# Kernel tuning notes

Measured on AMD Instinct MI355X. Metric: run time of the kernel, lower is better.

The kernel has to match this reference:

```python
import jax, jax.numpy as jnp
import numpy as np

EPS = 1e-06  # used both as eps and as the F.threshold threshold (mqjs passes eps as th)


def _pair_log_dist_sum(x1, x2, th):
    # dist[i,j] = ||x1_i||^2 + ||x2_j||^2 - 2 x1_i . x2_j  (n x n)
    x1x2 = x1 @ x2.T
    sq1 = jnp.sum(x1 * x1, axis=1)[:, None]
    sq2 = jnp.sum(x2 * x2, axis=1)[None, :]
    dist = sq1 + sq2 - 2.0 * x1x2
    # F.threshold(dist, th, 1): values <= th -> 1; then clamp(min=1), sqrt, log, row-sum
    dist = jnp.where(dist > th, dist, 1.0)
    dist = jnp.maximum(dist, 1.0)
    return jnp.sum(0.5 * jnp.log(dist), axis=1)  # log(sqrt(d)) == 0.5*log(d)


def _mqjs(inp, tgt, eps):
    n = inp.shape[0]
    x1 = inp.reshape(n, -1)
    x2 = tgt.reshape(n, -1)
    p = (x1 + x2) / 2.0
    ce = _pair_log_dist_sum(x1, p, eps) + _pair_log_dist_sum(x2, p, eps)
    se = _pair_log_dist_sum(x1, x1, eps) * (n / (n - 1))
    return jnp.mean(ce - se)


def setup_inputs() -> dict:
    key = jax.random.key(0)
    k1, k2 = jax.random.split(key)
    n, d = 8192, 256
    inp = jax.random.normal(k1, (n, d), dtype=jnp.float32)
    tgt = jax.random.normal(k2, (n, d), dtype=jnp.float32)
    return {"input": inp, "target": tgt}


def reference(input, target):
    return _mqjs(input, target, EPS)
```

## Files before the change

### kernel.cpp

```cpp
#include <hip/hip_runtime.h>

#define N 8192
#define D 256
#define BM 128
#define BJ 64
#define JG 4
#define GJ (N / BJ / JG)
#define GI (N / BM)

typedef int   i32x4 __attribute__((ext_vector_type(4)));
typedef int   i32x8 __attribute__((ext_vector_type(8)));
typedef float f32x4 __attribute__((ext_vector_type(4)));
typedef float f32x2 __attribute__((ext_vector_type(2)));

__device__ __forceinline__ unsigned pack_fp8x4(float a, float b, float c, float d) {
    unsigned lo = __builtin_amdgcn_cvt_pk_fp8_f32(a, b, 0, false);
    return __builtin_amdgcn_cvt_pk_fp8_f32(c, d, lo, true);
}
__device__ __forceinline__ float dequant_sumsq(unsigned q) {
    const float v0 = __builtin_amdgcn_cvt_f32_fp8(q, 0);
    const float v1 = __builtin_amdgcn_cvt_f32_fp8(q, 1);
    const float v2 = __builtin_amdgcn_cvt_f32_fp8(q, 2);
    const float v3 = __builtin_amdgcn_cvt_f32_fp8(q, 3);
    return fmaf(v0, v0, fmaf(v1, v1, fmaf(v2, v2, v3 * v3)));
}

__global__ void prep_kernel(const float* __restrict__ x1, const float* __restrict__ x2,
                            unsigned* __restrict__ x1q, unsigned* __restrict__ x2q,
                            unsigned* __restrict__ pq,
                            float* __restrict__ sq1, float* __restrict__ sq2,
                            float* __restrict__ sqp) {
    const int tid = threadIdx.x, lane = tid & 63, wv = tid >> 6;
    const int row = blockIdx.x * 4 + wv;
    const size_t eb = (size_t)row * D + lane * 4;
    const float4 a = *(const float4*)(x1 + eb);
    const float4 b = *(const float4*)(x2 + eb);
    const float px = 0.5f * (a.x + b.x), py = 0.5f * (a.y + b.y);
    const float pz = 0.5f * (a.z + b.z), pw = 0.5f * (a.w + b.w);
    const unsigned qa = pack_fp8x4(a.x, a.y, a.z, a.w);
    const unsigned qb = pack_fp8x4(b.x, b.y, b.z, b.w);
    const unsigned qp = pack_fp8x4(px, py, pz, pw);
    const size_t wb = (size_t)row * (D / 4) + lane;
    x1q[wb] = qa; x2q[wb] = qb; pq[wb] = qp;
    float s1 = dequant_sumsq(qa), s2 = dequant_sumsq(qb), sp = dequant_sumsq(qp);
    #pragma unroll
    for (int o = 32; o > 0; o >>= 1) {
        s1 += __shfl_down(s1, o, 64);
        s2 += __shfl_down(s2, o, 64);
        sp += __shfl_down(sp, o, 64);
    }
    if (lane == 0) { sq1[row] = s1; sq2[row] = s2; sqp[row] = sp; }
}

__device__ __forceinline__ f32x4 mfma8(i32x8 a, i32x8 b, f32x4 c) {
    return __builtin_amdgcn_mfma_scale_f32_16x16x128_f8f6f4(
        a, b, c, 0, 0, 0, 0x7F7F7F7F, 0, 0x7F7F7F7F);
}

__device__ __forceinline__ i32x8 frag_at(const unsigned char* b, int olo, int ohi) {
    const i32x4 lo = *(const i32x4*)(b + olo);
    const i32x4 hi = *(const i32x4*)(b + ohi);
    i32x8 f;
    f[0] = lo[0]; f[1] = lo[1]; f[2] = lo[2]; f[3] = lo[3];
    f[4] = hi[0]; f[5] = hi[1]; f[6] = hi[2]; f[7] = hi[3];
    return f;
}

__device__ __forceinline__ void stageB8(const unsigned char* __restrict__ g,
                                        unsigned char* s, int rowbase, size_t kb,
                                        int wv, int srow, int sblk) {
    const int row = wv * 8 + srow;
    __builtin_amdgcn_global_load_lds(
        (const __attribute__((address_space(1))) void*)(g + (size_t)(rowbase + row) * D + kb + sblk * 16),
        (__attribute__((address_space(3))) void*)(s + wv * 1024), 16, 0, 0);
}

__device__ __forceinline__ float logsumP(const f32x4 (&acc)[2][2],
                                         const f32x2 (&sa01)[2], const f32x2 (&sa23)[2],
                                         const float sb[2]) {
    float s = 0.0f;
    #pragma unroll
    for (int ti = 0; ti < 2; ++ti) {
        f32x2 pr = {1.0f, 1.0f};
        #pragma unroll
        for (int tj = 0; tj < 2; ++tj) {
            const f32x2 sbv = {sb[tj], sb[tj]};
            const f32x2 t01 = sa01[ti] + sbv, t23 = sa23[ti] + sbv;
            const f32x2 v01 = {acc[ti][tj][0], acc[ti][tj][1]};
            const f32x2 v23 = {acc[ti][tj][2], acc[ti][tj][3]};
            f32x2 d01 = t01 - 2.0f * v01;
            f32x2 d23 = t23 - 2.0f * v23;
            d01 = __builtin_elementwise_max(d01, (f32x2){1.0f, 1.0f});
            d23 = __builtin_elementwise_max(d23, (f32x2){1.0f, 1.0f});
            pr *= d01; pr *= d23;
        }
        s += __log2f(pr.x * pr.y);
    }
    return s;
}

__device__ __forceinline__ float logsumStraddle(const f32x4 (&acc)[2][2],
                                                const f32x2 (&sa01)[2], const f32x2 (&sa23)[2],
                                                const float sb[2],
                                                int wr, int wc, int quad, int l15,
                                                int I0, int J0) {
    float s = 0.0f;
    #pragma unroll
    for (int ti = 0; ti < 2; ++ti) {
        #pragma unroll
        for (int tj = 0; tj < 2; ++tj) {
            const int j = J0 + wc * 32 + tj * 16 + l15;
            float pr = 1.0f;
            #pragma unroll
            for (int r = 0; r < 4; ++r) {
                const int i = I0 + wr * 32 + ti * 16 + quad * 4 + r;
                const float sav = (r < 2) ? ((r & 1) ? sa01[ti].y : sa01[ti].x)
                                          : ((r & 1) ? sa23[ti].y : sa23[ti].x);
                float d = fmaf(-2.0f, acc[ti][tj][r], sav + sb[tj]);
                d = fmaxf(d, 1.0f);
                const float t = (j > i) ? d : 1.0f;
                const float u = (j >= i) ? d : 1.0f;
                pr *= t * u;
            }
            s += __log2f(pr);
        }
    }
    return s;
}

__global__ __launch_bounds__(512, 4) void mqjs_main(
    const unsigned char* __restrict__ x1q, const unsigned char* __restrict__ x2q,
    const unsigned char* __restrict__ pq,
    const float* __restrict__ sq1, const float* __restrict__ sq2,
    const float* __restrict__ sqp, float* __restrict__ partials) {

    __shared__ __align__(16) unsigned char Bs[JG * 16384];
    __shared__ float red[8];

    const int tid = threadIdx.x;
    const int lane = tid & 63;
    const int wv = tid >> 6;
    const int wr = wv >> 1, wc = wv & 1;
    const int quad = lane >> 4, l15 = lane & 15;
    const int srow = lane >> 3;
    const int sblk = (lane & 7) ^ srow;

    const int z = blockIdx.z;
    const int I0 = blockIdx.y * BM;
    const int jbase = blockIdx.x * JG;
    const int pid = (z * GI + blockIdx.y) * GJ + blockIdx.x;
    const float wse = -(float)N / (float)(N - 1);

    int jj0 = 0;
    if (z == 2) {
        jj0 = 2 * (int)blockIdx.y - jbase;
        if (jj0 < 0) jj0 = 0;
        if (jj0 >= JG) { if (tid == 0) partials[pid] = 0.0f; return; }
    }

    const unsigned char* Ag = (z == 1) ? x2q : x1q;
    const unsigned char* Bg = (z == 2) ? x1q : pq;
    const float* sqAg = (z == 1) ? sq2 : sq1;
    const float* sqBg = (z == 2) ? sq1 : sqp;

    for (int jj = jj0; jj < JG; ++jj) {
        stageB8(Bg, &Bs[jj * 16384],        (jbase + jj) * BJ, 0,   wv, srow, sblk);
        stageB8(Bg, &Bs[jj * 16384 + 8192], (jbase + jj) * BJ, 128, wv, srow, sblk);
    }

    i32x8 af[2][2];
    f32x2 sa01[2], sa23[2];
    #pragma unroll
    for (int ti = 0; ti < 2; ++ti) {
        #pragma unroll
        for (int kc = 0; kc < 2; ++kc) {
            const size_t ro = (size_t)(I0 + wr * 32 + ti * 16 + l15) * D + kc * 128 + quad * 32;
            af[kc][ti] = *(const i32x8*)(Ag + ro);
        }
        const int sbase = I0 + wr * 32 + ti * 16 + quad * 4;
        const float4 sv = *(const float4*)(sqAg + sbase);
        sa01[ti] = (f32x2){sv.x, sv.y};
        sa23[ti] = (f32x2){sv.z, sv.w};
    }

    asm volatile("s_waitcnt vmcnt(0)" ::: "memory");
    __syncthreads();

    const int m0 = wc * 32 + l15;
    const int r7 = m0 & 7;
    const int o0 = m0 * 128 + (((2 * quad)     ^ r7) << 4);
    const int o1 = m0 * 128 + (((2 * quad + 1) ^ r7) << 4);

    float tsum = 0.0f;
    const f32x4 zero4 = {0.0f, 0.0f, 0.0f, 0.0f};

    auto TILE = [&](int jj, f32x4 (&acc)[2][2], float (&sb)[2]) {
        const unsigned char* tb = &Bs[jj * 16384];
        const float* sp = sqBg + (jbase + jj) * BJ + m0;
        sb[0] = sp[0]; sb[1] = sp[16];
        __builtin_amdgcn_s_setprio(1);
        i32x8 b0 = frag_at(tb, o0, o1);
        i32x8 b1 = frag_at(tb + 2048, o0, o1);
        acc[0][0] = mfma8(af[0][0], b0, zero4);
        acc[0][1] = mfma8(af[0][0], b1, zero4);
        acc[1][0] = mfma8(af[0][1], b0, zero4);
        acc[1][1] = mfma8(af[0][1], b1, zero4);
        b0 = frag_at(tb + 8192, o0, o1);
        b1 = frag_at(tb + 8192 + 2048, o0, o1);
        acc[0][0] = mfma8(af[1][0], b0, acc[0][0]);
        acc[0][1] = mfma8(af[1][0], b1, acc[0][1]);
        acc[1][0] = mfma8(af[1][1], b0, acc[1][0]);
        acc[1][1] = mfma8(af[1][1], b1, acc[1][1]);
        __builtin_amdgcn_s_setprio(0);
    };

    auto EPI = [&](int jj, const f32x4 (&acc)[2][2], const float (&sb)[2]) {
        const int J0 = (jbase + jj) * BJ;
        if (z < 2) {
            tsum += 0.5f * logsumP(acc, sa01, sa23, sb);
        } else if (J0 >= I0 + BM) {
            tsum += wse * logsumP(acc, sa01, sa23, sb);
        } else {
            tsum += 0.5f * wse * logsumStraddle(acc, sa01, sa23, sb, wr, wc, quad, l15, I0, J0);
        }
    };

    f32x4 accA[2][2], accB[2][2];
    float sbA[2], sbB[2];

    if (jj0 == 0) {
        TILE(0, accA, sbA);
        TILE(1, accB, sbB); EPI(0, accA, sbA);
        TILE(2, accA, sbA); EPI(1, accB, sbB);
        TILE(3, accB, sbB); EPI(2, accA, sbA);
        EPI(3, accB, sbB);
    } else {
        TILE(jj0, accA, sbA);
        for (int jj = jj0 + 1; jj < JG; ++jj) {
            if (((jj - jj0) & 1) == 1) { TILE(jj, accB, sbB); EPI(jj - 1, accA, sbA); }
            else                       { TILE(jj, accA, sbA); EPI(jj - 1, accB, sbB); }
        }
        if (((JG - jj0) & 1) == 1) EPI(JG - 1, accA, sbA);
        else                       EPI(JG - 1, accB, sbB);
    }

    tsum *= 0.6931471805599453f;
    #pragma unroll
    for (int o = 32; o > 0; o >>= 1) tsum += __shfl_down(tsum, o, 64);
    if (lane == 0) red[wv] = tsum;
    __syncthreads();
    if (tid == 0) {
        float t = 0.0f;
        #pragma unroll
        for (int i = 0; i < 8; ++i) t += red[i];
        partials[pid] = t;
    }
}

__global__ void finalize_kernel(const float* __restrict__ partials, float* __restrict__ out) {
    const int tid = threadIdx.x;
    const float4 a = ((const float4*)partials)[tid];
    const float4 b = ((const float4*)partials)[tid + 768];
    double s = (double)a.x + (double)a.y + (double)a.z + (double)a.w
             + (double)b.x + (double)b.y + (double)b.z + (double)b.w;
    #pragma unroll
    for (int o = 32; o > 0; o >>= 1) s += __shfl_down(s, o, 64);
    __shared__ double r[12];
    if ((tid & 63) == 0) r[tid >> 6] = s;
    __syncthreads();
    if (tid == 0) {
        double t = 0.0;
        #pragma unroll
        for (int i = 0; i < 12; ++i) t += r[i];
        out[0] = (float)(t / (double)N);
    }
}

extern "C" void kernel_launch(void* const* d_in, const int* in_sizes, int n_in,
                              void* d_out, int out_size, void* d_ws, size_t ws_size,
                              hipStream_t stream) {
    const float* x1 = (const float*)d_in[0];
    const float* x2 = (const float*)d_in[1];

    char* ws = (char*)d_ws;
    const size_t MBYTES = (size_t)N * D;
    unsigned* x1q = (unsigned*)(ws);
    unsigned* x2q = (unsigned*)(ws + MBYTES);
    unsigned* pq  = (unsigned*)(ws + 2 * MBYTES);
    float* sq1 = (float*)(ws + 3 * MBYTES);
    float* sq2 = (float*)(ws + 3 * MBYTES + (size_t)N * 4);
    float* sqp = (float*)(ws + 3 * MBYTES + (size_t)N * 8);
    float* partials = (float*)(ws + 3 * MBYTES + (size_t)N * 12);

    prep_kernel<<<N / 4, 256, 0, stream>>>(x1, x2, x1q, x2q, pq, sq1, sq2, sqp);
    mqjs_main<<<dim3(GJ, GI, 3), 512, 0, stream>>>(
        (const unsigned char*)x1q, (const unsigned char*)x2q, (const unsigned char*)pq,
        sq1, sq2, sqp, partials);
    finalize_kernel<<<1, 768, 0, stream>>>(partials, (float*)d_out);
}
```

Measured before the change: 141.9 us.

## Reuse staged B tiles across four I row-blocks per workgroup

Each workgroup now covers four 128-row I blocks (IG=4) instead of one, so the B tiles staged in shared memory are reused across all of them and the grid shrinks by four, cutting LDS staging and global B traffic per unit of work. The software-pipelined TILE/EPI double-buffering is replaced by a plain sequential loop, with the triangular skip for the self-term done per tile. Fewer workgroups reduce parallelism and load balance on the triangular z=2 slice, and losing the MFMA/epilogue overlap may expose latency. The finalize kernel is resized to the smaller partials count.

New measurement: 132.2 us. 6.9% less time.

```diff
diff --git a/kernel.cpp b/kernel.cpp
--- a/kernel.cpp
+++ b/kernel.cpp
@@ -5,8 +5,10 @@
 #define BM 128
 #define BJ 64
 #define JG 4
-#define GJ (N / BJ / JG)
-#define GI (N / BM)
+#define IG 4
+#define GJP (N / (BJ * JG))
+#define GIG (N / (BM * IG))
+#define NPART (3 * GIG * GJP)
 
 typedef int   i32x4 __attribute__((ext_vector_type(4)));
 typedef int   i32x8 __attribute__((ext_vector_type(8)));
@@ -146,16 +148,15 @@
     const int sblk = (lane & 7) ^ srow;
 
     const int z = blockIdx.z;
-    const int I0 = blockIdx.y * BM;
     const int jbase = blockIdx.x * JG;
-    const int pid = (z * GI + blockIdx.y) * GJ + blockIdx.x;
+    const int Ibase = blockIdx.y * (BM * IG);
+    const int pid = (z * GIG + blockIdx.y) * GJP + blockIdx.x;
     const float wse = -(float)N / (float)(N - 1);
-
-    int jj0 = 0;
-    if (z == 2) {
-        jj0 = 2 * (int)blockIdx.y - jbase;
-        if (jj0 < 0) jj0 = 0;
-        if (jj0 >= JG) { if (tid == 0) partials[pid] = 0.0f; return; }
+    const int Jmax0 = (jbase + JG - 1) * BJ;
+
+    if (z == 2 && Jmax0 < Ibase) {
+        if (tid == 0) partials[pid] = 0.0f;
+        return;
     }
 
     const unsigned char* Ag = (z == 1) ? x2q : x1q;
@@ -163,24 +164,10 @@
     const float* sqAg = (z == 1) ? sq2 : sq1;
     const float* sqBg = (z == 2) ? sq1 : sqp;
 
-    for (int jj = jj0; jj < JG; ++jj) {
+    #pragma unroll
+    for (int jj = 0; jj < JG; ++jj) {
         stageB8(Bg, &Bs[jj * 16384],        (jbase + jj) * BJ, 0,   wv, srow, sblk);
         stageB8(Bg, &Bs[jj * 16384 + 8192], (jbase + jj) * BJ, 128, wv, srow, sblk);
-    }
-
-    i32x8 af[2][2];
-    f32x2 sa01[2], sa23[2];
-    #pragma unroll
-    for (int ti = 0; ti < 2; ++ti) {
-        #pragma unroll
-        for (int kc = 0; kc < 2; ++kc) {
-            const size_t ro = (size_t)(I0 + wr * 32 + ti * 16 + l15) * D + kc * 128 + quad * 32;
-            af[kc][ti] = *(const i32x8*)(Ag + ro);
-        }
-        const int sbase = I0 + wr * 32 + ti * 16 + quad * 4;
-        const float4 sv = *(const float4*)(sqAg + sbase);
-        sa01[ti] = (f32x2){sv.x, sv.y};
-        sa23[ti] = (f32x2){sv.z, sv.w};
     }
 
     asm volatile("s_waitcnt vmcnt(0)" ::: "memory");
@@ -194,54 +181,61 @@
     float tsum = 0.0f;
     const f32x4 zero4 = {0.0f, 0.0f, 0.0f, 0.0f};
 
-    auto TILE = [&](int jj, f32x4 (&acc)[2][2], float (&sb)[2]) {
-        const unsigned char* tb = &Bs[jj * 16384];
-        const float* sp = sqBg + (jbase + jj) * BJ + m0;
-        sb[0] = sp[0]; sb[1] = sp[16];
-        __builtin_amdgcn_s_setprio(1);
-        i32x8 b0 = frag_at(tb, o0, o1);
-        i32x8 b1 = frag_at(tb + 2048, o0, o1);
-        acc[0][0] = mfma8(af[0][0], b0, zero4);
-        acc[0][1] = mfma8(af[0][0], b1, zero4);
-        acc[1][0] = mfma8(af[0][1], b0, zero4);
-        acc[1][1] = mfma8(af[0][1], b1, zero4);
-        b0 = frag_at(tb + 8192, o0, o1);
-        b1 = frag_at(tb + 8192 + 2048, o0, o1);
-        acc[0][0] = mfma8(af[1][0], b0, acc[0][0]);
-        acc[0][1] = mfma8(af[1][0], b1, acc[0][1]);
-        acc[1][0] = mfma8(af[1][1], b0, acc[1][0]);
-        acc[1][1] = mfma8(af[1][1], b1, acc[1][1]);
-        __builtin_amdgcn_s_setprio(0);
-    };
-
-    auto EPI = [&](int jj, const f32x4 (&acc)[2][2], const float (&sb)[2]) {
-        const int J0 = (jbase + jj) * BJ;
-        if (z < 2) {
-            tsum += 0.5f * logsumP(acc, sa01, sa23, sb);
-        } else if (J0 >= I0 + BM) {
-            tsum += wse * logsumP(acc, sa01, sa23, sb);
-        } else {
-            tsum += 0.5f * wse * logsumStraddle(acc, sa01, sa23, sb, wr, wc, quad, l15, I0, J0);
-        }
-    };
-
-    f32x4 accA[2][2], accB[2][2];
-    float sbA[2], sbB[2];
-
-    if (jj0 == 0) {
-        TILE(0, accA, sbA);
-        TILE(1, accB, sbB); EPI(0, accA, sbA);
-        TILE(2, accA, sbA); EPI(1, accB, sbB);
-        TILE(3, accB, sbB); EPI(2, accA, sbA);
-        EPI(3, accB, sbB);
-    } else {
-        TILE(jj0, accA, sbA);
-        for (int jj = jj0 + 1; jj < JG; ++jj) {
-            if (((jj - jj0) & 1) == 1) { TILE(jj, accB, sbB); EPI(jj - 1, accA, sbA); }
-            else                       { TILE(jj, accA, sbA); EPI(jj - 1, accB, sbB); }
-        }
-        if (((JG - jj0) & 1) == 1) EPI(JG - 1, accA, sbA);
-        else                       EPI(JG - 1, accB, sbB);
+    #pragma unroll 1
+    for (int it = 0; it < IG; ++it) {
+        const int I0 = Ibase + it * BM;
+        if (z == 2 && Jmax0 < I0) continue;
+
+        i32x8 af[2][2];
+        f32x2 sa01[2], sa23[2];
+        #pragma unroll
+        for (int ti = 0; ti < 2; ++ti) {
+            #pragma unroll
+            for (int kc = 0; kc < 2; ++kc) {
+                const size_t ro = (size_t)(I0 + wr * 32 + ti * 16 + l15) * D + kc * 128 + quad * 32;
+                af[kc][ti] = *(const i32x8*)(Ag + ro);
+            }
+            const int sbase = I0 + wr * 32 + ti * 16 + quad * 4;
+            const float4 sv = *(const float4*)(sqAg + sbase);
+            sa01[ti] = (f32x2){sv.x, sv.y};
+            sa23[ti] = (f32x2){sv.z, sv.w};
+        }
+
+        #pragma unroll 1
+        for (int jj = 0; jj < JG; ++jj) {
+            const int J0 = (jbase + jj) * BJ;
+            if (z == 2 && J0 < I0) continue;
+
+            const unsigned char* tb = &Bs[jj * 16384];
+            const float* sp = sqBg + J0 + m0;
+            float sb[2];
+            sb[0] = sp[0]; sb[1] = sp[16];
+
+            f32x4 acc[2][2];
+            __builtin_amdgcn_s_setprio(1);
+            i32x8 b0 = frag_at(tb, o0, o1);
+            i32x8 b1 = frag_at(tb + 2048, o0, o1);
+            acc[0][0] = mfma8(af[0][0], b0, zero4);
+            acc[0][1] = mfma8(af[0][0], b1, zero4);
+            acc[1][0] = mfma8(af[0][1], b0, zero4);
+            acc[1][1] = mfma8(af[0][1], b1, zero4);
+            b0 = frag_at(tb + 8192, o0, o1);
+            b1 = frag_at(tb + 8192 + 2048, o0, o1);
+            acc[0][0] = mfma8(af[1][0], b0, acc[0][0]);
+            acc[0][1] = mfma8(af[1][0], b1, acc[0][1]);
+            acc[1][0] = mfma8(af[1][1], b0, acc[1][0]);
+            acc[1][1] = mfma8(af[1][1], b1, acc[1][1]);
+            __builtin_amdgcn_s_setprio(0);
+
+            if (z < 2) {
+                tsum += 0.5f * logsumP(acc, sa01, sa23, sb);
+            } else if (J0 >= I0 + BM) {
+                tsum += wse * logsumP(acc, sa01, sa23, sb);
+            } else {
+                tsum += 0.5f * wse * logsumStraddle(acc, sa01, sa23, sb,
+                                                    wr, wc, quad, l15, I0, J0);
+            }
+        }
     }
 
     tsum *= 0.6931471805599453f;
@@ -259,19 +253,17 @@
 
 __global__ void finalize_kernel(const float* __restrict__ partials, float* __restrict__ out) {
     const int tid = threadIdx.x;
-    const float4 a = ((const float4*)partials)[tid];
-    const float4 b = ((const float4*)partials)[tid + 768];
-    double s = (double)a.x + (double)a.y + (double)a.z + (double)a.w
-             + (double)b.x + (double)b.y + (double)b.z + (double)b.w;
+    const float4 v = ((const float4*)partials)[tid];
+    double s = (double)v.x + (double)v.y + (double)v.z + (double)v.w;
     #pragma unroll
     for (int o = 32; o > 0; o >>= 1) s += __shfl_down(s, o, 64);
-    __shared__ double r[12];
+    __shared__ double r[6];
     if ((tid & 63) == 0) r[tid >> 6] = s;
     __syncthreads();
     if (tid == 0) {
         double t = 0.0;
         #pragma unroll
-        for (int i = 0; i < 12; ++i) t += r[i];
+        for (int i = 0; i < 6; ++i) t += r[i];
         out[0] = (float)(t / (double)N);
     }
 }
@@ -293,8 +285,8 @@
     float* partials = (float*)(ws + 3 * MBYTES + (size_t)N * 12);
 
     prep_kernel<<<N / 4, 256, 0, stream>>>(x1, x2, x1q, x2q, pq, sq1, sq2, sqp);
-    mqjs_main<<<dim3(GJ, GI, 3), 512, 0, stream>>>(
+    mqjs_main<<<dim3(GJP, GIG, 3), 512, 0, stream>>>(
         (const unsigned char*)x1q, (const unsigned char*)x2q, (const unsigned char*)pq,
         sq1, sq2, sqp, partials);
-    finalize_kernel<<<1, 768, 0, stream>>>(partials, (float*)d_out);
-}
+    finalize_kernel<<<1, 384, 0, stream>>>(partials, (float*)d_out);
+}
```
